# Performance work log

Measured on AMD Instinct MI355X. Metric: run time of the kernel, lower is better.

The kernel has to match this reference:

```python
import jax, jax.numpy as jnp
import numpy as np

GRID = 3  # 3x3 grid; with H=W=168 and center_hw=56 all patches are 56x56


def setup_inputs() -> dict:
    key = jax.random.key(0)
    k1, k2, k3, k4 = jax.random.split(key, 4)
    B, C, H, W = 8, 256, 168, 168
    d = C // 8
    x = jax.random.normal(k1, (B, C, H, W), dtype=jnp.float32)
    W_B = jax.random.normal(k2, (d, C), dtype=jnp.float32) * 0.05
    W_D = jax.random.normal(k3, (d, C), dtype=jnp.float32) * 0.05
    W_phi = jax.random.normal(k4, (C, d), dtype=jnp.float32) * 0.05
    return {"x": x, "W_B": W_B, "W_D": W_D, "W_phi": W_phi}


def _psnl(fflat, W_B, W_D, W_phi):
    # fflat: [P, C, n] flattened patches; low-rank (non-softmax) path
    n = fflat.shape[-1]
    d = W_B.shape[0]
    Bn = jnp.einsum('dc,pcn->pnd', W_B, fflat)   # to_B, [P,n,d]
    Dn = jnp.einsum('dc,pcn->pnd', W_D, fflat)   # to_D
    Bc = Bn - jnp.mean(Bn, axis=1, keepdims=True)  # mean-center over positions
    T = jnp.einsum('pnd,pne->pde', Bc, Dn) / jnp.float32(n)  # [P,d,d]
    U = jnp.einsum('pnd,pde->pne', Bc, T)        # [P,n,d]
    out = jnp.einsum('cd,pnd->pcn', W_phi, U)    # phi 1x1 conv
    return out + fflat


def reference(x, W_B, W_D, W_phi):
    B, C, H, W = x.shape
    ph, pw = H // GRID, W // GRID
    n = ph * pw
    # split into 3x3 equal patches: [B,C,H,W] -> [B*9, C, n]
    xp = x.reshape(B, C, GRID, ph, GRID, pw)
    xp = xp.transpose(0, 2, 4, 1, 3, 5).reshape(B * GRID * GRID, C, n)
    yp = _psnl(xp, W_B, W_D, W_phi)
    # reassemble
    y = yp.reshape(B, GRID, GRID, C, ph, pw).transpose(0, 3, 1, 4, 2, 5)
    return y.reshape(B, C, H, W)
```

## Files before the change

### kernel.cpp

```cpp
#include <hip/hip_runtime.h>


#define BB    8
#define CC    256
#define HH    168
#define WWs   168
#define HWs   28224
#define PH    56
#define NPOS  3136
#define NP    72
#define DD    32
#define NPART 13

#define OFF_WBT 0
#define OFF_WDT (OFF_WBT + 8192)
#define OFF_BN  (OFF_WDT + 8192)
#define OFF_SP  (OFF_BN + 7225344)
#define OFF_MBP (OFF_SP + 958464)
#define OFF_MDP (OFF_MBP + 29952)
#define OFF_G   (OFF_MDP + 29952)
#define OFF_H   (OFF_G + 589824)

__global__ void ktrans(const float* __restrict__ wb, const float* __restrict__ wd,
                       float* __restrict__ wbt, float* __restrict__ wdt) {
    const int c = threadIdx.x;
    #pragma unroll
    for (int d = 0; d < DD; ++d) {
        wbt[c * DD + d] = wb[d * CC + c];
        wdt[c * DD + d] = wd[d * CC + c];
    }
}

__global__ __launch_bounds__(256, 4) void kAB(const float* __restrict__ x,
                                              const float* __restrict__ wbt,
                                              const float* __restrict__ wdt,
                                              float* __restrict__ bn,
                                              float* __restrict__ spart,
                                              float* __restrict__ mbp,
                                              float* __restrict__ mdp) {
    const int jb = blockIdx.x;
    const int p  = blockIdx.y;
    const int t  = threadIdx.x;
    const int j  = jb * 256 + t;
    const bool valid = j < NPOS;
    const int jc = valid ? j : (NPOS - 1);
    const int b  = p / 9;
    const int gy = (p % 9) / 3;
    const int gx = p % 3;
    const int iy = jc / PH;
    const int ix = jc % PH;
    const long base = (long)b * CC * HWs + (long)(gy * PH + iy) * WWs + (gx * PH + ix);

    float accB[DD], accD[DD];
    #pragma unroll
    for (int d = 0; d < DD; ++d) { accB[d] = 0.f; accD[d] = 0.f; }

    const float* xc = x + base;
    #pragma unroll 1
    for (int c0 = 0; c0 < CC; c0 += 8) {
        float xv[8];
        #pragma unroll
        for (int u = 0; u < 8; ++u) xv[u] = xc[(long)u * HWs];
        #pragma unroll
        for (int u = 0; u < 8; ++u) {
            const float* wbp = wbt + (c0 + u) * DD;
            const float* wdp = wdt + (c0 + u) * DD;
            #pragma unroll
            for (int d = 0; d < DD; ++d) {
                accB[d] = fmaf(xv[u], wbp[d], accB[d]);
                accD[d] = fmaf(xv[u], wdp[d], accD[d]);
            }
        }
        xc += 8L * HWs;
    }

    if (!valid) {
        #pragma unroll
        for (int d = 0; d < DD; ++d) { accB[d] = 0.f; accD[d] = 0.f; }
    } else {
        float* bp = bn + (long)p * DD * NPOS + j;
        #pragma unroll
        for (int d = 0; d < DD; ++d) bp[(long)d * NPOS] = accB[d];
    }

    __shared__ float Bt[128][33];
    __shared__ float Dt[128][33];
    const int d2 = (t >> 4) << 1;
    const int e2 = (t & 15) << 1;
    float a00 = 0, a01 = 0, a10 = 0, a11 = 0;
    float mb0 = 0, mb1 = 0, md0 = 0, md1 = 0;

    #pragma unroll 1
    for (int r = 0; r < 2; ++r) {
        __syncthreads();
        if ((t >> 7) == r) {
            const int tr = t & 127;
            #pragma unroll
            for (int d = 0; d < DD; ++d) {
                Bt[tr][d] = accB[d];
                Dt[tr][d] = accD[d];
            }
        }
        __syncthreads();
        #pragma unroll 4
        for (int jj = 0; jj < 128; ++jj) {
            const float2 bv = *(const float2*)&Bt[jj][d2];
            const float2 dv = *(const float2*)&Dt[jj][e2];
            a00 = fmaf(bv.x, dv.x, a00);
            a01 = fmaf(bv.x, dv.y, a01);
            a10 = fmaf(bv.y, dv.x, a10);
            a11 = fmaf(bv.y, dv.y, a11);
            if (e2 == 0) { mb0 += bv.x; mb1 += bv.y; }
            if (d2 == 0) { md0 += dv.x; md1 += dv.y; }
        }
    }

    float* sp = spart + (long)(p * NPART + jb) * 1024;
    sp[(d2    ) * DD + e2    ] = a00;
    sp[(d2    ) * DD + e2 + 1] = a01;
    sp[(d2 + 1) * DD + e2    ] = a10;
    sp[(d2 + 1) * DD + e2 + 1] = a11;
    if (e2 == 0) { mbp[(p * NPART + jb) * DD + d2] = mb0; mbp[(p * NPART + jb) * DD + d2 + 1] = mb1; }
    if (d2 == 0) { mdp[(p * NPART + jb) * DD + e2] = md0; mdp[(p * NPART + jb) * DD + e2 + 1] = md1; }
}

__global__ __launch_bounds__(256) void kB2(const float* __restrict__ wphi,
                                           const float* __restrict__ spart,
                                           const float* __restrict__ mbp,
                                           const float* __restrict__ mdp,
                                           float* __restrict__ gout,
                                           float* __restrict__ hout) {
    const int p = blockIdx.x;
    const int t = threadIdx.x;
    __shared__ float Tm[DD][DD + 1];
    __shared__ float mbs[DD], mds[DD];

    if (t < DD) {
        float s1 = 0, s2 = 0;
        for (int q = 0; q < NPART; ++q) {
            s1 += mbp[(p * NPART + q) * DD + t];
            s2 += mdp[(p * NPART + q) * DD + t];
        }
        mbs[t] = s1; mds[t] = s2;
    }
    __syncthreads();

    const float invn = 1.0f / (float)NPOS;
    {
        float4 s = make_float4(0.f, 0.f, 0.f, 0.f);
        for (int q = 0; q < NPART; ++q) {
            const float4 v = *(const float4*)&spart[(long)(p * NPART + q) * 1024 + t * 4];
            s.x += v.x; s.y += v.y; s.z += v.z; s.w += v.w;
        }
        const int idx = t * 4;
        const int d = idx >> 5;
        const int e = idx & 31;
        const float mbd = mbs[d] * invn;
        Tm[d][e    ] = s.x * invn - mbd * (mds[e    ] * invn);
        Tm[d][e + 1] = s.y * invn - mbd * (mds[e + 1] * invn);
        Tm[d][e + 2] = s.z * invn - mbd * (mds[e + 2] * invn);
        Tm[d][e + 3] = s.w * invn - mbd * (mds[e + 3] * invn);
    }
    __syncthreads();

    const int c = t;
    float wp[DD];
    #pragma unroll
    for (int e = 0; e < DD; ++e) wp[e] = wphi[c * DD + e];
    float h = 0.f;
    float* gp = gout + ((long)p * CC + c) * DD;
    #pragma unroll 4
    for (int d = 0; d < DD; ++d) {
        float g = 0.f;
        #pragma unroll
        for (int e = 0; e < DD; ++e) g = fmaf(wp[e], Tm[d][e], g);
        gp[d] = g;
        h = fmaf(mbs[d] * invn, g, h);
    }
    hout[p * CC + c] = h;
}

__global__ __launch_bounds__(256, 4) void kC(const float* __restrict__ x,
                                             const float* __restrict__ bn,
                                             const float* __restrict__ gbuf,
                                             const float* __restrict__ hbuf,
                                             float* __restrict__ out) {
    const int jb = blockIdx.x;
    const int p  = blockIdx.y;
    const int t  = threadIdx.x;
    const int j  = jb * 256 + t;
    const bool valid = j < NPOS;
    const int jc = valid ? j : (NPOS - 1);
    const int b  = p / 9;
    const int gy = (p % 9) / 3;
    const int gx = p % 3;
    const int iy = jc / PH;
    const int ix = jc % PH;
    const long base = (long)b * CC * HWs + (long)(gy * PH + iy) * WWs + (gx * PH + ix);

    float bnv[DD];
    const float* bp = bn + (long)p * DD * NPOS + jc;
    #pragma unroll
    for (int d = 0; d < DD; ++d) bnv[d] = bp[(long)d * NPOS];

    const float* gp = gbuf + (long)p * CC * DD;
    const float* hp = hbuf + p * CC;
    const float* xc = x + base;
    float* oc = out + base;
    #pragma unroll 1
    for (int c0 = 0; c0 < CC; c0 += 8) {
        float xv[8];
        #pragma unroll
        for (int u = 0; u < 8; ++u) xv[u] = xc[(long)u * HWs];
        #pragma unroll
        for (int u = 0; u < 8; ++u) {
            float acc = -hp[c0 + u];
            const float* g = gp + (c0 + u) * DD;
            #pragma unroll
            for (int d = 0; d < DD; ++d) acc = fmaf(bnv[d], g[d], acc);
            if (valid) oc[(long)u * HWs] = xv[u] + acc;
        }
        xc += 8L * HWs;
        oc += 8L * HWs;
    }
}

extern "C" void kernel_launch(void* const* d_in, const int* in_sizes, int n_in,
                              void* d_out, int out_size, void* d_ws, size_t ws_size,
                              hipStream_t stream) {
    const float* x    = (const float*)d_in[0];
    const float* wb   = (const float*)d_in[1];
    const float* wd   = (const float*)d_in[2];
    const float* wphi = (const float*)d_in[3];
    float* ws = (float*)d_ws;

    float* wbt = ws + OFF_WBT;
    float* wdt = ws + OFF_WDT;
    float* bnp = ws + OFF_BN;
    float* sp  = ws + OFF_SP;
    float* mbp = ws + OFF_MBP;
    float* mdp = ws + OFF_MDP;
    float* gb  = ws + OFF_G;
    float* hb  = ws + OFF_H;

    hipLaunchKernelGGL(ktrans, dim3(1), dim3(256), 0, stream, wb, wd, wbt, wdt);
    hipLaunchKernelGGL(kAB, dim3(13, 72), dim3(256), 0, stream, x, wbt, wdt, bnp, sp, mbp, mdp);
    hipLaunchKernelGGL(kB2, dim3(72), dim3(256), 0, stream, wphi, sp, mbp, mdp, gb, hb);
    hipLaunchKernelGGL(kC, dim3(13, 72), dim3(256), 0, stream, x, bnp, gb, hb, (float*)d_out);
}
```

Before: 584.8 us.

## Use bf16 MFMA for output projection with bf16 Bn and G buffers

Stores Bn and the fused G = W_phi·T matrix as bf16 in position-major layout, and replaces the scalar FMA output kernel with one that computes the rank-32 product per 16x16 tile using the bf16 MFMA intrinsic. It also halves the intermediate buffer traffic. Each block now covers 64 positions across all channels instead of 256 positions. The risks are lost precision from bf16 rounding and less coalesced output stores, since each lane writes scattered channel rows at 16-position granularity.

```diff
diff --git a/kernel.cpp b/kernel.cpp
--- a/kernel.cpp
+++ b/kernel.cpp
@@ -15,11 +15,19 @@
 #define OFF_WBT 0
 #define OFF_WDT (OFF_WBT + 8192)
 #define OFF_BN  (OFF_WDT + 8192)
-#define OFF_SP  (OFF_BN + 7225344)
+#define OFF_SP  (OFF_BN + 3612672)
 #define OFF_MBP (OFF_SP + 958464)
 #define OFF_MDP (OFF_MBP + 29952)
 #define OFF_G   (OFF_MDP + 29952)
-#define OFF_H   (OFF_G + 589824)
+#define OFF_H   (OFF_G + 294912)
+
+typedef __attribute__((ext_vector_type(8))) short short8v;
+typedef __attribute__((ext_vector_type(4))) float float4v;
+
+__device__ inline unsigned short f2bf(float f) {
+    unsigned int u = __float_as_uint(f);
+    return (unsigned short)((u + 0x7FFFu + ((u >> 16) & 1u)) >> 16);
+}
 
 __global__ void ktrans(const float* __restrict__ wb, const float* __restrict__ wd,
                        float* __restrict__ wbt, float* __restrict__ wdt) {
@@ -34,7 +42,7 @@
 __global__ __launch_bounds__(256, 4) void kAB(const float* __restrict__ x,
                                               const float* __restrict__ wbt,
                                               const float* __restrict__ wdt,
-                                              float* __restrict__ bn,
+                                              unsigned short* __restrict__ bn,
                                               float* __restrict__ spart,
                                               float* __restrict__ mbp,
                                               float* __restrict__ mdp) {
@@ -78,9 +86,14 @@
         #pragma unroll
         for (int d = 0; d < DD; ++d) { accB[d] = 0.f; accD[d] = 0.f; }
     } else {
-        float* bp = bn + (long)p * DD * NPOS + j;
-        #pragma unroll
-        for (int d = 0; d < DD; ++d) bp[(long)d * NPOS] = accB[d];
+        unsigned short* bp = bn + ((long)p * NPOS + j) * DD;
+        #pragma unroll
+        for (int d0 = 0; d0 < DD; d0 += 8) {
+            short8v v;
+            #pragma unroll
+            for (int i = 0; i < 8; ++i) v[i] = (short)f2bf(accB[d0 + i]);
+            *(short8v*)(bp + d0) = v;
+        }
     }
 
     __shared__ float Bt[128][33];
@@ -128,7 +141,7 @@
                                            const float* __restrict__ spart,
                                            const float* __restrict__ mbp,
                                            const float* __restrict__ mdp,
-                                           float* __restrict__ gout,
+                                           unsigned short* __restrict__ gout,
                                            float* __restrict__ hout) {
     const int p = blockIdx.x;
     const int t = threadIdx.x;
@@ -167,61 +180,73 @@
     float wp[DD];
     #pragma unroll
     for (int e = 0; e < DD; ++e) wp[e] = wphi[c * DD + e];
+    float gloc[DD];
     float h = 0.f;
-    float* gp = gout + ((long)p * CC + c) * DD;
-    #pragma unroll 4
+    #pragma unroll
     for (int d = 0; d < DD; ++d) {
         float g = 0.f;
         #pragma unroll
         for (int e = 0; e < DD; ++e) g = fmaf(wp[e], Tm[d][e], g);
-        gp[d] = g;
+        gloc[d] = g;
         h = fmaf(mbs[d] * invn, g, h);
     }
+    unsigned short* gp = gout + ((long)p * CC + c) * DD;
+    #pragma unroll
+    for (int d0 = 0; d0 < DD; d0 += 8) {
+        short8v v;
+        #pragma unroll
+        for (int i = 0; i < 8; ++i) v[i] = (short)f2bf(gloc[d0 + i]);
+        *(short8v*)(gp + d0) = v;
+    }
     hout[p * CC + c] = h;
 }
 
-__global__ __launch_bounds__(256, 4) void kC(const float* __restrict__ x,
-                                             const float* __restrict__ bn,
-                                             const float* __restrict__ gbuf,
-                                             const float* __restrict__ hbuf,
-                                             float* __restrict__ out) {
-    const int jb = blockIdx.x;
-    const int p  = blockIdx.y;
-    const int t  = threadIdx.x;
-    const int j  = jb * 256 + t;
-    const bool valid = j < NPOS;
-    const int jc = valid ? j : (NPOS - 1);
+__global__ __launch_bounds__(256, 4) void kCm(const float* __restrict__ x,
+                                              const unsigned short* __restrict__ bn,
+                                              const unsigned short* __restrict__ gbuf,
+                                              const float* __restrict__ hbuf,
+                                              float* __restrict__ out) {
+    const int jt   = blockIdx.x;
+    const int p    = blockIdx.y;
+    const int w    = threadIdx.x >> 6;
+    const int lane = threadIdx.x & 63;
     const int b  = p / 9;
     const int gy = (p % 9) / 3;
     const int gx = p % 3;
-    const int iy = jc / PH;
-    const int ix = jc % PH;
-    const long base = (long)b * CC * HWs + (long)(gy * PH + iy) * WWs + (gx * PH + ix);
-
-    float bnv[DD];
-    const float* bp = bn + (long)p * DD * NPOS + jc;
-    #pragma unroll
-    for (int d = 0; d < DD; ++d) bnv[d] = bp[(long)d * NPOS];
-
-    const float* gp = gbuf + (long)p * CC * DD;
-    const float* hp = hbuf + p * CC;
-    const float* xc = x + base;
-    float* oc = out + base;
-    #pragma unroll 1
-    for (int c0 = 0; c0 < CC; c0 += 8) {
-        float xv[8];
-        #pragma unroll
-        for (int u = 0; u < 8; ++u) xv[u] = xc[(long)u * HWs];
-        #pragma unroll
-        for (int u = 0; u < 8; ++u) {
-            float acc = -hp[c0 + u];
-            const float* g = gp + (c0 + u) * DD;
-            #pragma unroll
-            for (int d = 0; d < DD; ++d) acc = fmaf(bnv[d], g[d], acc);
-            if (valid) oc[(long)u * HWs] = xv[u] + acc;
-        }
-        xc += 8L * HWs;
-        oc += 8L * HWs;
+    const long xpatch = (long)b * CC * HWs + (long)(gy * PH) * WWs + gx * PH;
+
+    const int ln15 = lane & 15;
+    const int kslc = lane >> 4;
+
+    short8v bfr[4];
+    int joff[4];
+    const int jb64 = jt * 64;
+    #pragma unroll
+    for (int q = 0; q < 4; ++q) {
+        const int j = jb64 + q * 16 + ln15;
+        bfr[q] = *(const short8v*)(bn + ((long)p * NPOS + j) * DD + kslc * 8);
+        joff[q] = (j / PH) * WWs + (j % PH);
+    }
+
+    const int c0 = w * 64;
+    #pragma unroll
+    for (int ct = 0; ct < 4; ++ct) {
+        const int cb = c0 + ct * 16;
+        const short8v afr = *(const short8v*)(gbuf + ((long)p * CC + cb + ln15) * DD + kslc * 8);
+        float hv[4];
+        #pragma unroll
+        for (int r = 0; r < 4; ++r) hv[r] = hbuf[p * CC + cb + kslc * 4 + r];
+        #pragma unroll
+        for (int q = 0; q < 4; ++q) {
+            float4v acc = {0.f, 0.f, 0.f, 0.f};
+            acc = __builtin_amdgcn_mfma_f32_16x16x32_bf16(afr, bfr[q], acc, 0, 0, 0);
+            #pragma unroll
+            for (int r = 0; r < 4; ++r) {
+                const int c = cb + kslc * 4 + r;
+                const long addr = xpatch + (long)c * HWs + joff[q];
+                out[addr] = x[addr] + acc[r] - hv[r];
+            }
+        }
     }
 }
 
@@ -236,15 +261,15 @@
 
     float* wbt = ws + OFF_WBT;
     float* wdt = ws + OFF_WDT;
-    float* bnp = ws + OFF_BN;
+    unsigned short* bnp = (unsigned short*)(ws + OFF_BN);
     float* sp  = ws + OFF_SP;
     float* mbp = ws + OFF_MBP;
     float* mdp = ws + OFF_MDP;
-    float* gb  = ws + OFF_G;
+    unsigned short* gb = (unsigned short*)(ws + OFF_G);
     float* hb  = ws + OFF_H;
 
     hipLaunchKernelGGL(ktrans, dim3(1), dim3(256), 0, stream, wb, wd, wbt, wdt);
     hipLaunchKernelGGL(kAB, dim3(13, 72), dim3(256), 0, stream, x, wbt, wdt, bnp, sp, mbp, mdp);
     hipLaunchKernelGGL(kB2, dim3(72), dim3(256), 0, stream, wphi, sp, mbp, mdp, gb, hb);
-    hipLaunchKernelGGL(kC, dim3(13, 72), dim3(256), 0, stream, x, bnp, gb, hb, (float*)d_out);
-}
+    hipLaunchKernelGGL(kCm, dim3(49, 72), dim3(256), 0, stream, x, bnp, gb, hb, (float*)d_out);
+}
```

New measurement: 613.2 us. +4.8%, slower.
